# Performance work log

Measured on AMD Instinct MI355X. Metric: run time of the kernel, lower is better.

The kernel has to match this reference:

```python
import jax, jax.numpy as jnp
import numpy as np

N = 50000          # total_nodes (B*N diagonal-stacked graphs)
E = 800000         # total edges (avg degree 16)
HID = 128          # hidden_size
HEADS = 8          # num_heads


def setup_inputs() -> dict:
    key = jax.random.key(0)
    ks = jax.random.split(key, 10)
    s = 1.0 / np.sqrt(HID)
    x = jax.random.normal(ks[0], (N, HID), jnp.float32)
    edge_index = jax.random.randint(ks[1], (2, E), 0, N, dtype=jnp.int32).astype(jnp.int64)
    Wq = jax.random.normal(ks[2], (HID, HID), jnp.float32) * s
    bq = jax.random.normal(ks[3], (HID,), jnp.float32) * 0.01
    Wk = jax.random.normal(ks[4], (HID, HID), jnp.float32) * s
    bk = jax.random.normal(ks[5], (HID,), jnp.float32) * 0.01
    Wv = jax.random.normal(ks[6], (HID, HID), jnp.float32) * s
    bv = jax.random.normal(ks[7], (HID,), jnp.float32) * 0.01
    Wo = jax.random.normal(ks[8], (HID, HID), jnp.float32) * s
    bo = jax.random.normal(ks[9], (HID,), jnp.float32) * 0.01
    return {"x": x, "edge_index": edge_index, "total_nodes": N,
            "Wq": Wq, "bq": bq, "Wk": Wk, "bk": bk,
            "Wv": Wv, "bv": bv, "Wo": Wo, "bo": bo}


def reference(x, edge_index, total_nodes, Wq, bq, Wk, bk, Wv, bv, Wo, bo):
    H = HEADS
    D = HID // HEADS
    scale = D ** (-0.5)
    # torch Linear: y = x @ W.T + b
    Q = (x @ Wq.T + bq).reshape(-1, H, D)   # (N, H, D)
    K = (x @ Wk.T + bk).reshape(-1, H, D)
    V = (x @ Wv.T + bv).reshape(-1, H, D)
    src = edge_index[0]
    dst = edge_index[1]
    # edge-wise dot-product scores: (E, H)
    scores = jnp.einsum('ehd,ehd->eh', Q[dst], K[src]) * scale
    # scatter-softmax over edges sharing the same dst node
    mx = jax.ops.segment_max(scores, dst, num_segments=total_nodes)      # (N, H)
    ex = jnp.exp(scores - mx[dst])                                        # (E, H)
    se = jax.ops.segment_sum(ex, dst, num_segments=total_nodes)          # (N, H)
    attn = ex / (se[dst] + 1e-12)                                         # (E, H)
    # weighted message aggregation
    msg = attn[..., None] * V[src]                                        # (E, H, D)
    out = jax.ops.segment_sum(msg, dst, num_segments=total_nodes)        # (N, H, D)
    out = out.reshape(total_nodes, HID)
    return out @ Wo.T + bo
```

## Files before the change

### kernel.cpp

```cpp
#include <hip/hip_runtime.h>
#include <math.h>

#define NNODES 50000
#define NEDGES 800000
#define HIDDEN 128
#define NH 8
#define HD 16
#define CAP 64
#define NPART 8
#define PART_SZ 6250
#define SCAT_BPP 128
#define QKV_WAVES 6250

typedef __bf16 bf16x8 __attribute__((ext_vector_type(8)));
typedef float  f32x4  __attribute__((ext_vector_type(4)));

__device__ inline unsigned short f2b(float f) {
    unsigned u = __float_as_uint(f);
    unsigned r = (u + 0x7fffu + ((u >> 16) & 1u)) >> 16;
    return (unsigned short)r;
}

__device__ inline bf16x8 ld_a8(const float* __restrict__ p) {
    float4 a = *(const float4*)p;
    float4 b = *(const float4*)(p + 4);
    bf16x8 r;
    r[0] = (__bf16)a.x; r[1] = (__bf16)a.y; r[2] = (__bf16)a.z; r[3] = (__bf16)a.w;
    r[4] = (__bf16)b.x; r[5] = (__bf16)b.y; r[6] = (__bf16)b.z; r[7] = (__bf16)b.w;
    return r;
}

__global__ __launch_bounds__(256)
void pack_w(const float* __restrict__ Wq, const float* __restrict__ Wk,
            const float* __restrict__ Wv, const float* __restrict__ Wo,
            unsigned short* __restrict__ Pqkv, unsigned short* __restrict__ Po)
{
    const int s = blockIdx.x * 4 + (threadIdx.x >> 6);
    const int lane = threadIdx.x & 63;
    const float* W; unsigned short* P; int ct, c;
    if (s < 96) { ct = s >> 2; c = s & 3;
        W = (ct < 8) ? Wq : (ct < 16) ? Wk : Wv;
        P = Pqkv + (size_t)s * 512;
        ct &= 7;
    } else { int t = s - 96; ct = t >> 2; c = t & 3; W = Wo; P = Po + (size_t)t * 512; }
    const int colin = ct * 16 + (lane & 15);
    const int k0 = c * 32 + (lane >> 4) * 8;
    const float* sp = W + (size_t)colin * 128 + k0;
    unsigned short v[8];
#pragma unroll
    for (int j = 0; j < 8; ++j) v[j] = f2b(sp[j]);
    uint4 o;
    o.x = (unsigned)v[0] | ((unsigned)v[1] << 16);
    o.y = (unsigned)v[2] | ((unsigned)v[3] << 16);
    o.z = (unsigned)v[4] | ((unsigned)v[5] << 16);
    o.w = (unsigned)v[6] | ((unsigned)v[7] << 16);
    *(uint4*)(P + lane * 8) = o;
}

__global__ __launch_bounds__(256)
void scatter_kernel(const int* __restrict__ src, const int* __restrict__ dst,
                    int* __restrict__ cnt, int* __restrict__ bucket)
{
    const int part = blockIdx.x & (NPART - 1);
    const int blk  = blockIdx.x >> 3;
    const int lo = part * PART_SZ, hi = lo + PART_SZ;
    for (int e = blk * 256 + threadIdx.x; e < NEDGES; e += SCAT_BPP * 256) {
        const int d = dst[e];
        if (d >= lo && d < hi) {
            const int pos = atomicAdd(&cnt[d], 1);
            if (pos < CAP) bucket[d * CAP + pos] = src[e];
        }
    }
}

__global__ __launch_bounds__(256)
void qkv_mfma(const float* __restrict__ x, const unsigned short* __restrict__ Pqkv,
              const float* __restrict__ bq, const float* __restrict__ bk,
              const float* __restrict__ bv,
              unsigned short* __restrict__ Qb, unsigned short* __restrict__ KVb)
{
    const int w = blockIdx.x * 4 + (threadIdx.x >> 6);
    if (w >= QKV_WAVES) return;
    const int lane = threadIdx.x & 63;
    const int band = w >> 1, half = w & 1;
    const int row0 = band * 16;
    const int ar = lane & 15, kg = lane >> 4;

    const float* ap = x + (size_t)(row0 + ar) * 128 + kg * 8;
    const bf16x8 a0 = ld_a8(ap);
    const bf16x8 a1 = ld_a8(ap + 32);
    const bf16x8 a2 = ld_a8(ap + 64);
    const bf16x8 a3 = ld_a8(ap + 96);

    const unsigned short* wp = Pqkv + (size_t)(half * 48) * 512 + lane * 8;
    bf16x8 nb0 = *(const bf16x8*)(wp);
    bf16x8 nb1 = *(const bf16x8*)(wp + 512);
    bf16x8 nb2 = *(const bf16x8*)(wp + 1024);
    bf16x8 nb3 = *(const bf16x8*)(wp + 1536);

#pragma unroll
    for (int t = 0; t < 12; ++t) {
        const bf16x8 b0 = nb0, b1 = nb1, b2 = nb2, b3 = nb3;
        if (t < 11) {
            const unsigned short* nw = wp + (size_t)(t + 1) * 2048;
            nb0 = *(const bf16x8*)(nw);
            nb1 = *(const bf16x8*)(nw + 512);
            nb2 = *(const bf16x8*)(nw + 1024);
            nb3 = *(const bf16x8*)(nw + 1536);
        }
        f32x4 acc = {0.f, 0.f, 0.f, 0.f};
        acc = __builtin_amdgcn_mfma_f32_16x16x32_bf16(a0, b0, acc, 0, 0, 0);
        acc = __builtin_amdgcn_mfma_f32_16x16x32_bf16(a1, b1, acc, 0, 0, 0);
        acc = __builtin_amdgcn_mfma_f32_16x16x32_bf16(a2, b2, acc, 0, 0, 0);
        acc = __builtin_amdgcn_mfma_f32_16x16x32_bf16(a3, b3, acc, 0, 0, 0);

        const int ct = half * 12 + t;
        const int sel = ct >> 3;
        const int colin = (ct & 7) * 16 + ar;
        if (sel == 0) {
            const float bsc = bq[colin];
#pragma unroll
            for (int j = 0; j < 4; ++j)
                Qb[(size_t)(row0 + kg * 4 + j) * 128 + colin] = f2b(acc[j] + bsc);
        } else {
            const float bsc = (sel == 1) ? bk[colin] : bv[colin];
            const int koff = (sel == 2) ? 2 : 0;
            const int cbase = (colin >> 1) * 4 + (colin & 1) + koff;
#pragma unroll
            for (int j = 0; j < 4; ++j)
                KVb[(size_t)(row0 + kg * 4 + j) * 256 + cbase] = f2b(acc[j] + bsc);
        }
    }
}

__global__ __launch_bounds__(256)
void fused_attn_kernel(const unsigned short* __restrict__ Qb,
                       const unsigned short* __restrict__ KVb,
                       const int* __restrict__ cnt, const int* __restrict__ bucket,
                       unsigned short* __restrict__ accumb)
{
    const int wave = threadIdx.x >> 6;
    const int lane = threadIdx.x & 63;
    const int n = blockIdx.x * 4 + wave;
    if (n >= NNODES) return;

    int deg = cnt[n];
    deg = deg > CAP ? CAP : deg;
    const int mysrc = (lane < deg) ? bucket[n * CAP + lane] : 0;

    const unsigned short* kvbase = KVb + lane * 4;

    const unsigned qw = *(const unsigned*)(Qb + (size_t)n * HIDDEN + lane * 2);
    const float qx = __uint_as_float(qw << 16) * 0.25f;
    const float qy = __uint_as_float(qw & 0xffff0000u) * 0.25f;

    float m = -INFINITY, s = 0.f, ox = 0.f, oy = 0.f;

    uint2 kvA = make_uint2(0,0), kvB = kvA, kvC = kvA, kvD = kvA;
    if (deg > 0) kvA = *(const uint2*)(kvbase + ((size_t)__shfl(mysrc, 0) << 8));
    if (deg > 1) kvB = *(const uint2*)(kvbase + ((size_t)__shfl(mysrc, 1) << 8));
    if (deg > 2) kvC = *(const uint2*)(kvbase + ((size_t)__shfl(mysrc, 2) << 8));
    if (deg > 3) kvD = *(const uint2*)(kvbase + ((size_t)__shfl(mysrc, 3) << 8));

    int i = 0;
    for (; i + 2 <= deg; i += 2) {
        const uint2 c0 = kvA, c1 = kvB;
        kvA = kvC; kvB = kvD;
        if (i + 4 < deg) kvC = *(const uint2*)(kvbase + ((size_t)__shfl(mysrc, i + 4) << 8));
        if (i + 5 < deg) kvD = *(const uint2*)(kvbase + ((size_t)__shfl(mysrc, i + 5) << 8));

        float d0 = qx * __uint_as_float(c0.x << 16) + qy * __uint_as_float(c0.x & 0xffff0000u);
        float d1 = qx * __uint_as_float(c1.x << 16) + qy * __uint_as_float(c1.x & 0xffff0000u);
        d0 += __shfl_xor(d0, 1);  d1 += __shfl_xor(d1, 1);
        d0 += __shfl_xor(d0, 2);  d1 += __shfl_xor(d1, 2);
        d0 += __shfl_xor(d0, 4);  d1 += __shfl_xor(d1, 4);

        const float pm = fmaxf(d0, d1);
        const float ee = __expf(-fabsf(d0 - d1));
        const bool g = d0 >= d1;
        const float v0x = __uint_as_float(c0.y << 16), v0y = __uint_as_float(c0.y & 0xffff0000u);
        const float v1x = __uint_as_float(c1.y << 16), v1y = __uint_as_float(c1.y & 0xffff0000u);
        const float sp  = 1.f + ee;
        const float ovx = fmaf(ee, g ? v1x : v0x, g ? v0x : v1x);
        const float ovy = fmaf(ee, g ? v1y : v0y, g ? v0y : v1y);

        const float dd = pm - m;
        const float em = __expf(-fabsf(dd));
        const bool nm = dd > 0.f;
        const float so = nm ? em : 1.f;
        const float sn = nm ? 1.f : em;
        m = nm ? pm : m;
        s  = fmaf(s,  so, sp  * sn);
        ox = fmaf(ox, so, ovx * sn);
        oy = fmaf(oy, so, ovy * sn);
    }
    if (i < deg) {
        const uint2 c0 = kvA;
        float d0 = qx * __uint_as_float(c0.x << 16) + qy * __uint_as_float(c0.x & 0xffff0000u);
        d0 += __shfl_xor(d0, 1);
        d0 += __shfl_xor(d0, 2);
        d0 += __shfl_xor(d0, 4);
        const float vx = __uint_as_float(c0.y << 16), vy = __uint_as_float(c0.y & 0xffff0000u);
        const float dd = d0 - m;
        const float em = __expf(-fabsf(dd));
        const bool nm = dd > 0.f;
        const float so = nm ? em : 1.f;
        const float pp = nm ? 1.f : em;
        m = nm ? d0 : m;
        s  = fmaf(s,  so, pp);
        ox = fmaf(ox, so, pp * vx);
        oy = fmaf(oy, so, pp * vy);
    }
    const float inv = 1.f / (s + 1e-12f);
    ushort2 ob = { f2b(ox * inv), f2b(oy * inv) };
    *(ushort2*)(accumb + (size_t)n * HIDDEN + lane * 2) = ob;
}

__global__ __launch_bounds__(256)
void outproj_mfma(const unsigned short* __restrict__ accumb, const unsigned short* __restrict__ Po,
                  const float* __restrict__ bo, float* __restrict__ out)
{
    const int band = blockIdx.x * 4 + (threadIdx.x >> 6);
    if (band >= 3125) return;
    const int lane = threadIdx.x & 63;
    const int row0 = band * 16;
    const int ar = lane & 15, kg = lane >> 4;

    const unsigned short* ab = accumb + (size_t)(row0 + ar) * 128 + kg * 8;
    const bf16x8 a0 = *(const bf16x8*)(ab);
    const bf16x8 a1 = *(const bf16x8*)(ab + 32);
    const bf16x8 a2 = *(const bf16x8*)(ab + 64);
    const bf16x8 a3 = *(const bf16x8*)(ab + 96);

    const unsigned short* wp = Po + lane * 8;
    bf16x8 nb0 = *(const bf16x8*)(wp);
    bf16x8 nb1 = *(const bf16x8*)(wp + 512);
    bf16x8 nb2 = *(const bf16x8*)(wp + 1024);
    bf16x8 nb3 = *(const bf16x8*)(wp + 1536);

#pragma unroll
    for (int t = 0; t < 8; ++t) {
        const bf16x8 b0 = nb0, b1 = nb1, b2 = nb2, b3 = nb3;
        if (t < 7) {
            const unsigned short* nw = wp + (size_t)(t + 1) * 2048;
            nb0 = *(const bf16x8*)(nw);
            nb1 = *(const bf16x8*)(nw + 512);
            nb2 = *(const bf16x8*)(nw + 1024);
            nb3 = *(const bf16x8*)(nw + 1536);
        }
        f32x4 acc = {0.f, 0.f, 0.f, 0.f};
        acc = __builtin_amdgcn_mfma_f32_16x16x32_bf16(a0, b0, acc, 0, 0, 0);
        acc = __builtin_amdgcn_mfma_f32_16x16x32_bf16(a1, b1, acc, 0, 0, 0);
        acc = __builtin_amdgcn_mfma_f32_16x16x32_bf16(a2, b2, acc, 0, 0, 0);
        acc = __builtin_amdgcn_mfma_f32_16x16x32_bf16(a3, b3, acc, 0, 0, 0);

        const int colin = t * 16 + ar;
        const float bsc = bo[colin];
#pragma unroll
        for (int j = 0; j < 4; ++j)
            out[(size_t)(row0 + kg * 4 + j) * 128 + colin] = acc[j] + bsc;
    }
}

extern "C" void kernel_launch(void* const* d_in, const int* in_sizes, int n_in,
                              void* d_out, int out_size, void* d_ws, size_t ws_size,
                              hipStream_t stream) {
    const float* x  = (const float*)d_in[0];
    const int*   ei = (const int*)d_in[1];
    const int*   src = ei;
    const int*   dst = ei + NEDGES;
    const float* Wq = (const float*)d_in[3];
    const float* bq = (const float*)d_in[4];
    const float* Wk = (const float*)d_in[5];
    const float* bk = (const float*)d_in[6];
    const float* Wv = (const float*)d_in[7];
    const float* bv = (const float*)d_in[8];
    const float* Wo = (const float*)d_in[9];
    const float* bo = (const float*)d_in[10];
    float* out = (float*)d_out;

    char* ws = (char*)d_ws;
    size_t off = 0;
    const size_t sz_nhb = (size_t)NNODES * HIDDEN * sizeof(unsigned short);
    unsigned short* Qb     = (unsigned short*)(ws + off); off += sz_nhb;
    unsigned short* KVb    = (unsigned short*)(ws + off); off += 2 * sz_nhb;
    unsigned short* accumb = (unsigned short*)(ws + off); off += sz_nhb;
    unsigned short* Pqkv   = (unsigned short*)(ws + off); off += 96 * 512 * sizeof(unsigned short);
    unsigned short* Po     = (unsigned short*)(ws + off); off += 32 * 512 * sizeof(unsigned short);
    int*            cnt    = (int*)(ws + off);            off += (size_t)NNODES * sizeof(int);
    int*            bucket = (int*)(ws + off);            off += (size_t)NNODES * CAP * sizeof(int);

    hipMemsetAsync(cnt, 0, (size_t)NNODES * sizeof(int), stream);

    pack_w<<<32, 256, 0, stream>>>(Wq, Wk, Wv, Wo, Pqkv, Po);

    scatter_kernel<<<NPART * SCAT_BPP, 256, 0, stream>>>(src, dst, cnt, bucket);

    qkv_mfma<<<(QKV_WAVES + 3) / 4, 256, 0, stream>>>(x, Pqkv, bq, bk, bv, Qb, KVb);

    fused_attn_kernel<<<(NNODES + 3) / 4, 256, 0, stream>>>(Qb, KVb, cnt, bucket, accumb);

    outproj_mfma<<<782, 256, 0, stream>>>(accumb, Po, bo, out);
}
```

Measured before the change: 147.9 us.

## Fuse counter zeroing into weight packing and merge QKV GEMM with edge scatter

Replaces the memset with extra blocks in the weight-packing kernel that zero the per-node counters. The QKV projection and the edge bucketing scatter are merged into one launch, with block ranges picking the role. The two independent workloads can then run concurrently on the GPU, and two launches plus their gaps are removed. The cost is a heavier combined kernel whose resource use is set by the QKV path, and scatter blocks are scheduled after the QKV blocks.

```diff
diff --git a/kernel.cpp b/kernel.cpp
--- a/kernel.cpp
+++ b/kernel.cpp
@@ -10,7 +10,9 @@
 #define NPART 8
 #define PART_SZ 6250
 #define SCAT_BPP 128
+#define SCAT_BLOCKS (NPART * SCAT_BPP)
 #define QKV_WAVES 6250
+#define QKV_BLOCKS 1563
 
 typedef __bf16 bf16x8 __attribute__((ext_vector_type(8)));
 typedef float  f32x4  __attribute__((ext_vector_type(4)));
@@ -31,10 +33,16 @@
 }
 
 __global__ __launch_bounds__(256)
-void pack_w(const float* __restrict__ Wq, const float* __restrict__ Wk,
-            const float* __restrict__ Wv, const float* __restrict__ Wo,
-            unsigned short* __restrict__ Pqkv, unsigned short* __restrict__ Po)
+void pack_init(const float* __restrict__ Wq, const float* __restrict__ Wk,
+               const float* __restrict__ Wv, const float* __restrict__ Wo,
+               unsigned short* __restrict__ Pqkv, unsigned short* __restrict__ Po,
+               int* __restrict__ cnt)
 {
+    if (blockIdx.x >= 32) {
+        const int idx = (blockIdx.x - 32) * 256 + threadIdx.x;
+        if (idx < NNODES / 4) ((int4*)cnt)[idx] = make_int4(0, 0, 0, 0);
+        return;
+    }
     const int s = blockIdx.x * 4 + (threadIdx.x >> 6);
     const int lane = threadIdx.x & 63;
     const float* W; unsigned short* P; int ct, c;
@@ -58,27 +66,28 @@
 }
 
 __global__ __launch_bounds__(256)
-void scatter_kernel(const int* __restrict__ src, const int* __restrict__ dst,
-                    int* __restrict__ cnt, int* __restrict__ bucket)
+void qkv_scatter(const float* __restrict__ x, const unsigned short* __restrict__ Pqkv,
+                 const float* __restrict__ bq, const float* __restrict__ bk,
+                 const float* __restrict__ bv,
+                 const int* __restrict__ src, const int* __restrict__ dst,
+                 unsigned short* __restrict__ Qb, unsigned short* __restrict__ KVb,
+                 int* __restrict__ cnt, int* __restrict__ bucket)
 {
-    const int part = blockIdx.x & (NPART - 1);
-    const int blk  = blockIdx.x >> 3;
-    const int lo = part * PART_SZ, hi = lo + PART_SZ;
-    for (int e = blk * 256 + threadIdx.x; e < NEDGES; e += SCAT_BPP * 256) {
-        const int d = dst[e];
-        if (d >= lo && d < hi) {
-            const int pos = atomicAdd(&cnt[d], 1);
-            if (pos < CAP) bucket[d * CAP + pos] = src[e];
+    if (blockIdx.x >= QKV_BLOCKS) {
+        const int sb = blockIdx.x - QKV_BLOCKS;
+        const int part = sb & (NPART - 1);
+        const int blk  = sb >> 3;
+        const int lo = part * PART_SZ, hi = lo + PART_SZ;
+        for (int e = blk * 256 + threadIdx.x; e < NEDGES; e += SCAT_BPP * 256) {
+            const int d = dst[e];
+            if (d >= lo && d < hi) {
+                const int pos = atomicAdd(&cnt[d], 1);
+                if (pos < CAP) bucket[d * CAP + pos] = src[e];
+            }
         }
-    }
-}
-
-__global__ __launch_bounds__(256)
-void qkv_mfma(const float* __restrict__ x, const unsigned short* __restrict__ Pqkv,
-              const float* __restrict__ bq, const float* __restrict__ bk,
-              const float* __restrict__ bv,
-              unsigned short* __restrict__ Qb, unsigned short* __restrict__ KVb)
-{
+        return;
+    }
+
     const int w = blockIdx.x * 4 + (threadIdx.x >> 6);
     if (w >= QKV_WAVES) return;
     const int lane = threadIdx.x & 63;
@@ -290,13 +299,10 @@
     int*            cnt    = (int*)(ws + off);            off += (size_t)NNODES * sizeof(int);
     int*            bucket = (int*)(ws + off);            off += (size_t)NNODES * CAP * sizeof(int);
 
-    hipMemsetAsync(cnt, 0, (size_t)NNODES * sizeof(int), stream);
-
-    pack_w<<<32, 256, 0, stream>>>(Wq, Wk, Wv, Wo, Pqkv, Po);
-
-    scatter_kernel<<<NPART * SCAT_BPP, 256, 0, stream>>>(src, dst, cnt, bucket);
-
-    qkv_mfma<<<(QKV_WAVES + 3) / 4, 256, 0, stream>>>(x, Pqkv, bq, bk, bv, Qb, KVb);
+    pack_init<<<81, 256, 0, stream>>>(Wq, Wk, Wv, Wo, Pqkv, Po, cnt);
+
+    qkv_scatter<<<QKV_BLOCKS + SCAT_BLOCKS, 256, 0, stream>>>(
+        x, Pqkv, bq, bk, bv, src, dst, Qb, KVb, cnt, bucket);
 
     fused_attn_kernel<<<(NNODES + 3) / 4, 256, 0, stream>>>(Qb, KVb, cnt, bucket, accumb);
 
```

Measured after the change: 139.2 us. 1.06x faster.
